# Kernel optimization log

Hardware: AMD Instinct MI355X
Metric: run time of the kernel (lower is better)

## Reference

```python
import jax, jax.numpy as jnp
import numpy as np

EMBED_DIM = 768
NUM_HEADS = 12
PROJ_DIM = EMBED_DIM // NUM_HEADS
B, S = 8, 512
PRIOR_VAR = 0.01
LOG_PRIOR_VAR = float(np.log(PRIOR_VAR))


def _kl_regularizer(w_mu, w_sigma):
    # kl_loss broadcasts [in,units] mu against [units] logvar, then mean over all
    kl_loss = (LOG_PRIOR_VAR - 1.0 - w_sigma
               + jnp.log1p(jnp.exp(w_sigma)) / PRIOR_VAR
               + jnp.square(w_mu) / PRIOR_VAR)
    return 0.5 * jnp.mean(kl_loss)


def _linear_not_first(mu_in, Sigma_in, w_mu, w_sigma):
    in_dim = jnp.float32(w_mu.shape[0])
    units = jnp.float32(w_mu.shape[1])
    x_dim = jnp.float32(mu_in.shape[-1])
    mu_out = mu_in @ w_mu
    kl = _kl_regularizer(w_mu, w_sigma)
    W_Sigma = jnp.log1p(jnp.exp(w_sigma))  # softplus, shape [units]
    # w_t_Sigma_i_w: (w_mu/sqrt(in_dim))^2 = w_mu^2/in_dim
    Sigma_1 = Sigma_in @ (jnp.square(w_mu) / in_dim)
    # x_Sigma_w_x_T: x/x_dim, then sum(x*x) * W_Sigma
    xs = mu_in / x_dim
    xx_t = jnp.sum(xs * xs, axis=-1, keepdims=True)
    Sigma_2 = xx_t * W_Sigma
    # tr_Sigma_w_Sigma_in
    Sigma_3 = jnp.sum(Sigma_in, axis=-1, keepdims=True) * W_Sigma / units
    Sigma_out = jax.nn.softplus(Sigma_1 + Sigma_2 + Sigma_3)
    return mu_out, Sigma_out, kl


def _separate_heads(x):
    # [B,S,E] -> [B,H,S,d]
    return x.reshape(B, S, NUM_HEADS, PROJ_DIM).transpose(0, 2, 1, 3)


def _attention(mu_q, sg_q, mu_k, sg_k, mu_v, sg_v):
    dk = jnp.float32(PROJ_DIM)
    mu_score = jnp.einsum('bhqd,bhkd->bhqk', mu_q, mu_k)
    a = jnp.einsum('bhqd,bhkd->bhqk', jnp.square(mu_q) / dk, sg_k)
    # NOTE: faithful to TF source: matmul(mu_key^2/dk, sigma_query, transpose_b)
    b = jnp.einsum('bhkd,bhqd->bhkq', jnp.square(mu_k) / dk, sg_q)
    c = jnp.einsum('bhqd,bhkd->bhqk', sg_q, sg_k) / dk
    sigma_score = a + b + c
    mu_scaled = mu_score / jnp.sqrt(dk)
    sigma_scaled = sigma_score / dk
    mu_w = jax.nn.softmax(mu_scaled, axis=-1)
    wd = jnp.float32(mu_w.shape[-1])
    grad = jnp.square(mu_w - jnp.square(mu_w))
    Sigma_w = grad * sigma_scaled / wd
    mu_out = jnp.einsum('bhqk,bhkd->bhqd', mu_w, mu_v)
    d = jnp.einsum('bhqk,bhkd->bhqd', jnp.square(mu_w) / wd, sg_v)
    e = jnp.einsum('bhqk,bhkd->bhqd', Sigma_w, jnp.square(mu_v) / wd)
    f = jnp.einsum('bhqk,bhkd->bhqd', Sigma_w, sg_v) / wd
    return mu_out, jax.nn.softplus(d + e + f)


def _forward(mu_inputs, sigma_inputs, wq_mu, wq_sigma, wk_mu, wk_sigma,
             wv_mu, wv_sigma, wo_mu, wo_sigma):
    # eval mode: VDP_Dropout is identity
    mu_q, sg_q, kl_q = _linear_not_first(mu_inputs, sigma_inputs, wq_mu, wq_sigma)
    mu_k, sg_k, kl_k = _linear_not_first(mu_inputs, sigma_inputs, wk_mu, wk_sigma)
    mu_v, sg_v, kl_v = _linear_not_first(mu_inputs, sigma_inputs, wv_mu, wv_sigma)
    mu_q, sg_q = _separate_heads(mu_q), _separate_heads(sg_q)
    mu_k, sg_k = _separate_heads(mu_k), _separate_heads(sg_k)
    mu_v, sg_v = _separate_heads(mu_v), _separate_heads(sg_v)
    mu_att, sg_att = _attention(mu_q, sg_q, mu_k, sg_k, mu_v, sg_v)
    mu_cat = mu_att.transpose(0, 2, 1, 3).reshape(B, S, EMBED_DIM)
    sg_cat = sg_att.transpose(0, 2, 1, 3).reshape(B, S, EMBED_DIM)
    mu_out, Sigma_out, kl_o = _linear_not_first(mu_cat, sg_cat, wo_mu, wo_sigma)
    kl = kl_q + kl_k + kl_v + kl_o
    return mu_out, Sigma_out, kl


def setup_inputs() -> dict:
    key = jax.random.key(0)
    ks = jax.random.split(key, 10)
    glorot = float(np.sqrt(2.0 / (EMBED_DIM + EMBED_DIM)))
    def w_pair(k1, k2):
        w_mu = jax.random.normal(k1, (EMBED_DIM, EMBED_DIM), jnp.float32) * glorot
        w_sigma = jax.random.uniform(k2, (EMBED_DIM,), jnp.float32,
                                     minval=-4.6, maxval=-2.25)
        return w_mu, w_sigma
    wq_mu, wq_sigma = w_pair(ks[0], ks[1])
    wk_mu, wk_sigma = w_pair(ks[2], ks[3])
    wv_mu, wv_sigma = w_pair(ks[4], ks[5])
    wo_mu, wo_sigma = w_pair(ks[6], ks[7])
    mu_inputs = jax.random.normal(ks[8], (B, S, EMBED_DIM), jnp.float32)
    sigma_inputs = jax.random.uniform(ks[9], (B, S, EMBED_DIM), jnp.float32)
    return {"mu_inputs": mu_inputs, "sigma_inputs": sigma_inputs,
            "wq_mu": wq_mu, "wq_sigma": wq_sigma,
            "wk_mu": wk_mu, "wk_sigma": wk_sigma,
            "wv_mu": wv_mu, "wv_sigma": wv_sigma,
            "wo_mu": wo_mu, "wo_sigma": wo_sigma}


def reference(mu_inputs, sigma_inputs, wq_mu, wq_sigma, wk_mu, wk_sigma,
              wv_mu, wv_sigma, wo_mu, wo_sigma):
    return _forward(mu_inputs, sigma_inputs, wq_mu, wq_sigma, wk_mu, wk_sigma,
                    wv_mu, wv_sigma, wo_mu, wo_sigma)
```

## Files before the change

### kernel.cpp

```cpp
#include <hip/hip_runtime.h>
#include <math.h>

constexpr int E = 768;
constexpr int H = 12;
constexpr int D = 64;
constexpr int Bsz = 8;
constexpr int S = 512;
constexpr int NROWS = Bsz * S;
constexpr float LOG_PV_M1 = -5.605170185988091f;
constexpr float INV_PV = 100.0f;

typedef __attribute__((ext_vector_type(8))) short short8;
typedef __attribute__((ext_vector_type(4))) float floatx4;

__device__ __forceinline__ float softplusf(float x) {
    return fmaxf(x, 0.f) + log1pf(expf(-fabsf(x)));
}
__device__ __forceinline__ unsigned short f2bf(float f) {
    unsigned int u = __float_as_uint(f);
    unsigned int r = (u + 0x7fffu + ((u >> 16) & 1u)) >> 16;
    return (unsigned short)r;
}
__device__ __forceinline__ float bf2f(unsigned short h) {
    return __uint_as_float(((unsigned int)h) << 16);
}
__device__ __forceinline__ unsigned int pack2(float a, float b) {
    return (unsigned int)f2bf(a) | ((unsigned int)f2bf(b) << 16);
}
__device__ __forceinline__ void split2(float a, float b, unsigned int& hi, unsigned int& lo) {
    unsigned short ha = f2bf(a), hb = f2bf(b);
    hi = (unsigned int)ha | ((unsigned int)hb << 16);
    lo = (unsigned int)f2bf(a - bf2f(ha)) | ((unsigned int)f2bf(b - bf2f(hb)) << 16);
}

__global__ void zero_kernel(float* p) { if (threadIdx.x == 0) p[0] = 0.f; }

__global__ __launch_bounds__(256) void kl_kernel(const float* __restrict__ wmu,
                                                 const float* __restrict__ wsig,
                                                 float* __restrict__ out) {
    int tid = blockIdx.x * 256 + threadIdx.x;
    int nthr = gridDim.x * 256;
    float partial = 0.f;
    for (int i = tid; i < E * E; i += nthr) {
        float w = wmu[i];
        partial += w * w;
    }
    partial *= INV_PV;
    if (tid < E) {
        float ws = wsig[tid];
        partial += (float)E * (LOG_PV_M1 - ws + softplusf(ws) * INV_PV);
    }
    __shared__ float red[256];
    red[threadIdx.x] = partial;
    __syncthreads();
    for (int s = 128; s > 0; s >>= 1) {
        if (threadIdx.x < s) red[threadIdx.x] += red[threadIdx.x + s];
        __syncthreads();
    }
    if (threadIdx.x == 0)
        atomicAdd(out, 0.5f * red[0] / (float)(E * E));
}

__global__ __launch_bounds__(256) void rowstats_kernel(const float* __restrict__ mu,
                                                       const float* __restrict__ sg,
                                                       float* __restrict__ xx,
                                                       float* __restrict__ ss) {
    int wave = threadIdx.x >> 6, lane = threadIdx.x & 63;
    int row = blockIdx.x * 4 + wave;
    const float* mrow = mu + (size_t)row * E;
    const float* srow = sg + (size_t)row * E;
    float s2 = 0.f, s1 = 0.f;
    for (int i = lane; i < E; i += 64) {
        float m = mrow[i];
        s2 += m * m;
        s1 += srow[i];
    }
    for (int off = 32; off > 0; off >>= 1) {
        s2 += __shfl_xor(s2, off);
        s1 += __shfl_xor(s1, off);
    }
    if (lane == 0) {
        xx[row] = s2 * (1.f / ((float)E * (float)E));
        ss[row] = s1;
    }
}

__global__ __launch_bounds__(512, 1) void linear_mfma_kernel(
    const float* __restrict__ Amu, const float* __restrict__ Asg,
    const float* __restrict__ Wmu, const float* __restrict__ wsig,
    const float* __restrict__ xx, const float* __restrict__ ss,
    float* __restrict__ Cmu, float* __restrict__ Csg) {
    constexpr int BM = 64, BN = 128, BK = 32, LDK = 40;
    __shared__ unsigned short A_mu[BM][LDK], A_sg[BM][LDK];
    __shared__ unsigned short W_mu[BN][LDK], W_sg[BN][LDK];
    const int m0 = blockIdx.x * BM;
    const int n0 = blockIdx.y * BN;
    const int t = threadIdx.x;
    const int lane = t & 63, wid = t >> 6;
    const int qsub = wid >> 1, c2 = wid & 1;
    const int lr = lane & 15, lg = lane >> 4;

    floatx4 accm[4] = {{0.f,0.f,0.f,0.f},{0.f,0.f,0.f,0.f},{0.f,0.f,0.f,0.f},{0.f,0.f,0.f,0.f}};
    floatx4 accs[4] = {{0.f,0.f,0.f,0.f},{0.f,0.f,0.f,0.f},{0.f,0.f,0.f,0.f},{0.f,0.f,0.f,0.f}};

    for (int k0 = 0; k0 < E; k0 += BK) {
        __syncthreads();
        {
            int r = t >> 3, g = (t & 7) * 4;
            float4 am = *(const float4*)&Amu[(size_t)(m0 + r) * E + k0 + g];
            float4 as = *(const float4*)&Asg[(size_t)(m0 + r) * E + k0 + g];
            *(uint2*)&A_mu[r][g] = make_uint2(pack2(am.x, am.y), pack2(am.z, am.w));
            *(uint2*)&A_sg[r][g] = make_uint2(pack2(as.x, as.y), pack2(as.z, as.w));
        }
        {
            int kp = t & 15, n4 = (t >> 4) * 4;
            const float* p0 = &Wmu[(size_t)(k0 + 2 * kp) * E + n0 + n4];
            const float* p1 = p0 + E;
            float4 w0 = *(const float4*)p0, w1 = *(const float4*)p1;
            *(unsigned int*)&W_mu[n4 + 0][2 * kp] = pack2(w0.x, w1.x);
            *(unsigned int*)&W_mu[n4 + 1][2 * kp] = pack2(w0.y, w1.y);
            *(unsigned int*)&W_mu[n4 + 2][2 * kp] = pack2(w0.z, w1.z);
            *(unsigned int*)&W_mu[n4 + 3][2 * kp] = pack2(w0.w, w1.w);
            const float is = 1.f / 768.f;
            *(unsigned int*)&W_sg[n4 + 0][2 * kp] = pack2(w0.x * w0.x * is, w1.x * w1.x * is);
            *(unsigned int*)&W_sg[n4 + 1][2 * kp] = pack2(w0.y * w0.y * is, w1.y * w1.y * is);
            *(unsigned int*)&W_sg[n4 + 2][2 * kp] = pack2(w0.z * w0.z * is, w1.z * w1.z * is);
            *(unsigned int*)&W_sg[n4 + 3][2 * kp] = pack2(w0.w * w0.w * is, w1.w * w1.w * is);
        }
        __syncthreads();
        short8 a_mu = *(const short8*)&A_mu[qsub * 16 + lr][lg * 8];
        short8 a_sg = *(const short8*)&A_sg[qsub * 16 + lr][lg * 8];
#pragma unroll
        for (int f = 0; f < 4; ++f) {
            int col = c2 * 64 + f * 16 + lr;
            short8 b_mu = *(const short8*)&W_mu[col][lg * 8];
            short8 b_sg = *(const short8*)&W_sg[col][lg * 8];
            accm[f] = __builtin_amdgcn_mfma_f32_16x16x32_bf16(a_mu, b_mu, accm[f], 0, 0, 0);
            accs[f] = __builtin_amdgcn_mfma_f32_16x16x32_bf16(a_sg, b_sg, accs[f], 0, 0, 0);
        }
    }
#pragma unroll
    for (int f = 0; f < 4; ++f) {
        int n = n0 + c2 * 64 + f * 16 + lr;
        float WS = softplusf(wsig[n]);
#pragma unroll
        for (int v = 0; v < 4; ++v) {
            int m = m0 + qsub * 16 + lg * 4 + v;
            Cmu[(size_t)m * E + n] = accm[f][v];
            float sg = accs[f][v] + xx[m] * WS + ss[m] * WS * (1.f / 768.f);
            Csg[(size_t)m * E + n] = softplusf(sg);
        }
    }
}

__global__ __launch_bounds__(512, 1) void attn_mfma_kernel(
    const float* __restrict__ mu_q, const float* __restrict__ sg_q,
    const float* __restrict__ mu_k, const float* __restrict__ sg_k,
    const float* __restrict__ mu_v, const float* __restrict__ sg_v,
    float* __restrict__ mu_o, float* __restrict__ sg_o) {
    constexpr int QB = 64, KC = 64, LDK = 72;
    __shared__ unsigned short q_hi[QB][LDK], q_lo[QB][LDK], q_cb[QB][LDK], q_k2[QB][LDK];
    __shared__ unsigned short k_hi[KC][LDK], k_lo[KC][LDK], k_sg[KC][LDK], k_qsg[KC][LDK];
    __shared__ unsigned short vT_mu[D][LDK], vT_sg[D][LDK], vT_cb[D][LDK];
    __shared__ unsigned short p_w[QB][LDK], p_w2[QB][LDK], p_sw[QB][LDK];
    __shared__ float red_m[2][QB], red_z[2][QB];

    const int bid = blockIdx.x;
    const int qt = bid & 7;
    const int hb = bid >> 3;
    const int h = hb % H;
    const int b = hb / H;
    const int q0 = qt * QB;
    const int t = threadIdx.x;
    const int lane = t & 63, wid = t >> 6;
    const int qsub = wid >> 1, c2 = wid & 1;
    const int Q0 = qsub * 16;
    const int lr = lane & 15, lg = lane >> 4;
    const size_t base = (size_t)b * S * E + (size_t)h * D;

    {
        int r = t >> 3, g = (t & 7) * 8;
        const float* pm = mu_q + base + (size_t)(q0 + r) * E + g;
        const float* ps = sg_q + base + (size_t)(q0 + r) * E + g;
        const float* pk = mu_k + base + (size_t)(q0 + r) * E + g;
        float4 m0 = *(const float4*)pm, m1 = *(const float4*)(pm + 4);
        float4 s0 = *(const float4*)ps, s1 = *(const float4*)(ps + 4);
        float4 k0 = *(const float4*)pk, k1 = *(const float4*)(pk + 4);
        unsigned int h0, l0, h1, l1, h2, l2, h3, l3;
        split2(m0.x, m0.y, h0, l0); split2(m0.z, m0.w, h1, l1);
        split2(m1.x, m1.y, h2, l2); split2(m1.z, m1.w, h3, l3);
        *(uint4*)&q_hi[r][g] = make_uint4(h0, h1, h2, h3);
        *(uint4*)&q_lo[r][g] = make_uint4(l0, l1, l2, l3);
        const float i64 = 1.f / 64.f;
        *(uint4*)&q_cb[r][g] = make_uint4(
            pack2((m0.x * m0.x + s0.x) * i64, (m0.y * m0.y + s0.y) * i64),
            pack2((m0.z * m0.z + s0.z) * i64, (m0.w * m0.w + s0.w) * i64),
            pack2((m1.x * m1.x + s1.x) * i64, (m1.y * m1.y + s1.y) * i64),
            pack2((m1.z * m1.z + s1.z) * i64, (m1.w * m1.w + s1.w) * i64));
        *(uint4*)&q_k2[r][g] = make_uint4(
            pack2(k0.x * k0.x * i64, k0.y * k0.y * i64),
            pack2(k0.z * k0.z * i64, k0.w * k0.w * i64),
            pack2(k1.x * k1.x * i64, k1.y * k1.y * i64),
            pack2(k1.z * k1.z * i64, k1.w * k1.w * i64));
    }

    float mv[4], zv[4];
#pragma unroll
    for (int v = 0; v < 4; ++v) { mv[v] = -1e30f; zv[v] = 0.f; }

    for (int c = 0; c < S / KC; ++c) {
        __syncthreads();
        {
            int r = t >> 3, g = (t & 7) * 8;
            const float* pk = mu_k + base + (size_t)(c * KC + r) * E + g;
            float4 k0 = *(const float4*)pk, k1 = *(const float4*)(pk + 4);
            unsigned int h0, l0, h1, l1, h2, l2, h3, l3;
            split2(k0.x, k0.y, h0, l0); split2(k0.z, k0.w, h1, l1);
            split2(k1.x, k1.y, h2, l2); split2(k1.z, k1.w, h3, l3);
            *(uint4*)&k_hi[r][g] = make_uint4(h0, h1, h2, h3);
            *(uint4*)&k_lo[r][g] = make_uint4(l0, l1, l2, l3);
        }
        __syncthreads();
        floatx4 cm[2] = {{0.f, 0.f, 0.f, 0.f}, {0.f, 0.f, 0.f, 0.f}};
#pragma unroll
        for (int ks = 0; ks < 2; ++ks) {
            int ao = lg * 8 + ks * 32;
            short8 ahi = *(const short8*)&q_hi[Q0 + lr][ao];
            short8 alo = *(const short8*)&q_lo[Q0 + lr][ao];
#pragma unroll
            for (int f = 0; f < 2; ++f) {
                int key = c2 * 32 + f * 16 + lr;
                short8 bhi = *(const short8*)&k_hi[key][ao];
                short8 blo = *(const short8*)&k_lo[key][ao];
                cm[f] = __builtin_amdgcn_mfma_f32_16x16x32_bf16(ahi, bhi, cm[f], 0, 0, 0);
                cm[f] = __builtin_amdgcn_mfma_f32_16x16x32_bf16(ahi, blo, cm[f], 0, 0, 0);
                cm[f] = __builtin_amdgcn_mfma_f32_16x16x32_bf16(alo, bhi, cm[f], 0, 0, 0);
            }
        }
#pragma unroll
        for (int v = 0; v < 4; ++v) {
            float s0 = cm[0][v] * 0.125f, s1 = cm[1][v] * 0.125f;
            float cmx = fmaxf(s0, s1);
            for (int off = 1; off <= 8; off <<= 1) cmx = fmaxf(cmx, __shfl_xor(cmx, off));
            float ez = __expf(s0 - cmx) + __expf(s1 - cmx);
            for (int off = 1; off <= 8; off <<= 1) ez += __shfl_xor(ez, off);
            float nm = fmaxf(mv[v], cmx);
            zv[v] = zv[v] * __expf(mv[v] - nm) + ez * __expf(cmx - nm);
            mv[v] = nm;
        }
    }
    __syncthreads();
    if ((lane & 15) == 0) {
#pragma unroll
        for (int v = 0; v < 4; ++v) {
            int qr = Q0 + lg * 4 + v;
            red_m[c2][qr] = mv[v];
            red_z[c2][qr] = zv[v];
        }
    }
    __syncthreads();
    float fm[4], fzi[4];
#pragma unroll
    for (int v = 0; v < 4; ++v) {
        int qr = Q0 + lg * 4 + v;
        float m0 = red_m[0][qr], m1 = red_m[1][qr];
        float mm = fmaxf(m0, m1);
        float zz = red_z[0][qr] * __expf(m0 - mm) + red_z[1][qr] * __expf(m1 - mm);
        fm[v] = mm;
        fzi[v] = 1.f / zz;
    }

    floatx4 accm[2] = {{0.f, 0.f, 0.f, 0.f}, {0.f, 0.f, 0.f, 0.f}};
    floatx4 accs[2] = {{0.f, 0.f, 0.f, 0.f}, {0.f, 0.f, 0.f, 0.f}};
    for (int c = 0; c < S / KC; ++c) {
        __syncthreads();
        {
            int r = t >> 3, g = (t & 7) * 8;
            const float* pk = mu_k + base + (size_t)(c * KC + r) * E + g;
            const float* pskk = sg_k + base + (size_t)(c * KC + r) * E + g;
            const float* psq = sg_q + base + (size_t)(c * KC + r) * E + g;
            float4 k0 = *(const float4*)pk, k1 = *(const float4*)(pk + 4);
            float4 s0 = *(const float4*)pskk, s1 = *(const float4*)(pskk + 4);
            float4 g0 = *(const float4*)psq, g1 = *(const float4*)(psq + 4);
            unsigned int h0, l0, h1, l1, h2, l2, h3, l3;
            split2(k0.x, k0.y, h0, l0); split2(k0.z, k0.w, h1, l1);
            split2(k1.x, k1.y, h2, l2); split2(k1.z, k1.w, h3, l3);
            *(uint4*)&k_hi[r][g] = make_uint4(h0, h1, h2, h3);
            *(uint4*)&k_lo[r][g] = make_uint4(l0, l1, l2, l3);
            *(uint4*)&k_sg[r][g] = make_uint4(pack2(s0.x, s0.y), pack2(s0.z, s0.w),
                                              pack2(s1.x, s1.y), pack2(s1.z, s1.w));
            *(uint4*)&k_qsg[r][g] = make_uint4(pack2(g0.x, g0.y), pack2(g0.z, g0.w),
                                               pack2(g1.x, g1.y), pack2(g1.z, g1.w));
        }
        {
            int kp = t & 31, dg = (t >> 5) * 4;
            const float* pv0 = mu_v + base + (size_t)(c * KC + 2 * kp) * E + dg;
            const float* pv1 = pv0 + E;
            const float* ps0 = sg_v + base + (size_t)(c * KC + 2 * kp) * E + dg;
            const float* ps1 = ps0 + E;
            float4 a0 = *(const float4*)pv0, a1 = *(const float4*)pv1;
            float4 b0 = *(const float4*)ps0, b1 = *(const float4*)ps1;
            *(unsigned int*)&vT_mu[dg + 0][2 * kp] = pack2(a0.x, a1.x);
            *(unsigned int*)&vT_mu[dg + 1][2 * kp] = pack2(a0.y, a1.y);
            *(unsigned int*)&vT_mu[dg + 2][2 * kp] = pack2(a0.z, a1.z);
            *(unsigned int*)&vT_mu[dg + 3][2 * kp] = pack2(a0.w, a1.w);
            *(unsigned int*)&vT_sg[dg + 0][2 * kp] = pack2(b0.x, b1.x);
            *(unsigned int*)&vT_sg[dg + 1][2 * kp] = pack2(b0.y, b1.y);
            *(unsigned int*)&vT_sg[dg + 2][2 * kp] = pack2(b0.z, b1.z);
            *(unsigned int*)&vT_sg[dg + 3][2 * kp] = pack2(b0.w, b1.w);
            *(unsigned int*)&vT_cb[dg + 0][2 * kp] = pack2(a0.x * a0.x + b0.x, a1.x * a1.x + b1.x);
            *(unsigned int*)&vT_cb[dg + 1][2 * kp] = pack2(a0.y * a0.y + b0.y, a1.y * a1.y + b1.y);
            *(unsigned int*)&vT_cb[dg + 2][2 * kp] = pack2(a0.z * a0.z + b0.z, a1.z * a1.z + b1.z);
            *(unsigned int*)&vT_cb[dg + 3][2 * kp] = pack2(a0.w * a0.w + b0.w, a1.w * a1.w + b1.w);
        }
        __syncthreads();
        floatx4 cm[2] = {{0.f, 0.f, 0.f, 0.f}, {0.f, 0.f, 0.f, 0.f}};
        floatx4 cs[2] = {{0.f, 0.f, 0.f, 0.f}, {0.f, 0.f, 0.f, 0.f}};
#pragma unroll
        for (int ks = 0; ks < 2; ++ks) {
            int ao = lg * 8 + ks * 32;
            short8 ahi = *(const short8*)&q_hi[Q0 + lr][ao];
            short8 alo = *(const short8*)&q_lo[Q0 + lr][ao];
            short8 acb = *(const short8*)&q_cb[Q0 + lr][ao];
            short8 ak2 = *(const short8*)&q_k2[Q0 + lr][ao];
#pragma unroll
            for (int f = 0; f < 2; ++f) {
                int key = c2 * 32 + f * 16 + lr;
                short8 bhi = *(const short8*)&k_hi[key][ao];
                short8 blo = *(const short8*)&k_lo[key][ao];
                short8 bsg = *(const short8*)&k_sg[key][ao];
                short8 bqs = *(const short8*)&k_qsg[key][ao];
                cm[f] = __builtin_amdgcn_mfma_f32_16x16x32_bf16(ahi, bhi, cm[f], 0, 0, 0);
                cm[f] = __builtin_amdgcn_mfma_f32_16x16x32_bf16(ahi, blo, cm[f], 0, 0, 0);
                cm[f] = __builtin_amdgcn_mfma_f32_16x16x32_bf16(alo, bhi, cm[f], 0, 0, 0);
                cs[f] = __builtin_amdgcn_mfma_f32_16x16x32_bf16(acb, bsg, cs[f], 0, 0, 0);
                cs[f] = __builtin_amdgcn_mfma_f32_16x16x32_bf16(ak2, bqs, cs[f], 0, 0, 0);
            }
        }
#pragma unroll
        for (int f = 0; f < 2; ++f)
#pragma unroll
            for (int v = 0; v < 4; ++v) {
                int qr = Q0 + lg * 4 + v;
                int key = c2 * 32 + f * 16 + lr;
                float w = __expf(cm[f][v] * 0.125f - fm[v]) * fzi[v];
                float sgs = cs[f][v] * (1.f / 64.f);
                float g1 = w - w * w;
                p_w[qr][key] = f2bf(w);
                p_w2[qr][key] = f2bf(w * w * (1.f / 512.f));
                p_sw[qr][key] = f2bf(g1 * g1 * sgs * (1.f / 262144.f));
            }
        __syncthreads();
#pragma unroll
        for (int ks = 0; ks < 2; ++ks) {
            int ko = lg * 8 + ks * 32;
            short8 aw = *(const short8*)&p_w[Q0 + lr][ko];
            short8 aw2 = *(const short8*)&p_w2[Q0 + lr][ko];
            short8 asw = *(const short8*)&p_sw[Q0 + lr][ko];
#pragma unroll
            for (int nf = 0; nf < 2; ++nf) {
                int dcol = (wid & 1) * 32 + nf * 16 + lr;
                short8 bvm = *(const short8*)&vT_mu[dcol][ko];
                short8 bvs = *(const short8*)&vT_sg[dcol][ko];
                short8 bvc = *(const short8*)&vT_cb[dcol][ko];
                accm[nf] = __builtin_amdgcn_mfma_f32_16x16x32_bf16(aw, bvm, accm[nf], 0, 0, 0);
                accs[nf] = __builtin_amdgcn_mfma_f32_16x16x32_bf16(aw2, bvs, accs[nf], 0, 0, 0);
                accs[nf] = __builtin_amdgcn_mfma_f32_16x16x32_bf16(asw, bvc, accs[nf], 0, 0, 0);
            }
        }
    }
#pragma unroll
    for (int nf = 0; nf < 2; ++nf)
#pragma unroll
        for (int v = 0; v < 4; ++v) {
            int qg = q0 + Q0 + lg * 4 + v;
            int dcol = (wid & 1) * 32 + nf * 16 + lr;
            size_t g = base + (size_t)qg * E + dcol;
            mu_o[g] = accm[nf][v];
            sg_o[g] = softplusf(accs[nf][v]);
        }
}

extern "C" void kernel_launch(void* const* d_in, const int* in_sizes, int n_in,
                              void* d_out, int out_size, void* d_ws, size_t ws_size,
                              hipStream_t stream) {
    const float* mu_in = (const float*)d_in[0];
    const float* sg_in = (const float*)d_in[1];
    const float* wq_mu = (const float*)d_in[2];
    const float* wq_sg = (const float*)d_in[3];
    const float* wk_mu = (const float*)d_in[4];
    const float* wk_sg = (const float*)d_in[5];
    const float* wv_mu = (const float*)d_in[6];
    const float* wv_sg = (const float*)d_in[7];
    const float* wo_mu = (const float*)d_in[8];
    const float* wo_sg = (const float*)d_in[9];

    float* out_mu = (float*)d_out;
    float* out_sg = out_mu + (size_t)NROWS * E;
    float* out_kl = out_sg + (size_t)NROWS * E;

    const size_t NE = (size_t)NROWS * E;
    float* ws = (float*)d_ws;
    float* mu_q = ws;
    float* sg_q = ws + NE;
    float* mu_k = ws + 2 * NE;
    float* sg_k = ws + 3 * NE;
    float* mu_v = ws + 4 * NE;
    float* sg_v = ws + 5 * NE;
    float* mu_a = ws + 6 * NE;
    float* sg_a = ws + 7 * NE;
    float* xx = ws + 8 * NE;
    float* ss = xx + NROWS;
    float* xx2 = ss + NROWS;
    float* ss2 = xx2 + NROWS;

    zero_kernel<<<1, 64, 0, stream>>>(out_kl);
    kl_kernel<<<64, 256, 0, stream>>>(wq_mu, wq_sg, out_kl);
    kl_kernel<<<64, 256, 0, stream>>>(wk_mu, wk_sg, out_kl);
    kl_kernel<<<64, 256, 0, stream>>>(wv_mu, wv_sg, out_kl);
    kl_kernel<<<64, 256, 0, stream>>>(wo_mu, wo_sg, out_kl);

    rowstats_kernel<<<NROWS / 4, 256, 0, stream>>>(mu_in, sg_in, xx, ss);

    dim3 ggrid(NROWS / 64, E / 128);
    linear_mfma_kernel<<<ggrid, 512, 0, stream>>>(mu_in, sg_in, wq_mu, wq_sg, xx, ss, mu_q, sg_q);
    linear_mfma_kernel<<<ggrid, 512, 0, stream>>>(mu_in, sg_in, wk_mu, wk_sg, xx, ss, mu_k, sg_k);
    linear_mfma_kernel<<<ggrid, 512, 0, stream>>>(mu_in, sg_in, wv_mu, wv_sg, xx, ss, mu_v, sg_v);

    attn_mfma_kernel<<<Bsz * H * (S / 64), 512, 0, stream>>>(mu_q, sg_q, mu_k, sg_k,
                                                             mu_v, sg_v, mu_a, sg_a);

    rowstats_kernel<<<NROWS / 4, 256, 0, stream>>>(mu_a, sg_a, xx2, ss2);
    linear_mfma_kernel<<<ggrid, 512, 0, stream>>>(mu_a, sg_a, wo_mu, wo_sg, xx2, ss2, out_mu, out_sg);
}
```

Baseline: 540.4 us.

## Pre-pack inputs, weights and intermediates to bf16 in producer epilogues

Inputs and transposed weights (plus squared/scaled weight variants) are converted to bf16 once in dedicated pack kernels. The Q/K/V linear epilogues now write attention-ready bf16 planes (hi/lo splits, sigma, mu^2+sigma), and attention writes bf16 outputs consumed by a bf16 rowstats and the output projection. This is meant to halve intermediate memory traffic and remove repeated conversion and transposition work inside the GEMM and attention inner loops. In exchange it adds extra launches and storage of more planes, and the output projection now reads bf16-rounded attention outputs, which may reduce accuracy slightly.

```diff
diff --git a/kernel.cpp b/kernel.cpp
--- a/kernel.cpp
+++ b/kernel.cpp
@@ -7,6 +7,8 @@
 constexpr int Bsz = 8;
 constexpr int S = 512;
 constexpr int NROWS = Bsz * S;
+constexpr int NE_ = NROWS * E;
+constexpr int WE = E * E;
 constexpr float LOG_PV_M1 = -5.605170185988091f;
 constexpr float INV_PV = 100.0f;
 
@@ -26,11 +28,6 @@
 }
 __device__ __forceinline__ unsigned int pack2(float a, float b) {
     return (unsigned int)f2bf(a) | ((unsigned int)f2bf(b) << 16);
-}
-__device__ __forceinline__ void split2(float a, float b, unsigned int& hi, unsigned int& lo) {
-    unsigned short ha = f2bf(a), hb = f2bf(b);
-    hi = (unsigned int)ha | ((unsigned int)hb << 16);
-    lo = (unsigned int)f2bf(a - bf2f(ha)) | ((unsigned int)f2bf(b - bf2f(hb)) << 16);
 }
 
 __global__ void zero_kernel(float* p) { if (threadIdx.x == 0) p[0] = 0.f; }
@@ -59,6 +56,49 @@
     }
     if (threadIdx.x == 0)
         atomicAdd(out, 0.5f * red[0] / (float)(E * E));
+}
+
+__global__ __launch_bounds__(256) void pack_in_kernel(const float* __restrict__ mu,
+                                                      const float* __restrict__ sg,
+                                                      unsigned short* __restrict__ m16,
+                                                      unsigned short* __restrict__ s16) {
+    size_t i = ((size_t)blockIdx.x * 256 + threadIdx.x) * 8;
+    float4 a0 = *(const float4*)(mu + i);
+    float4 a1 = *(const float4*)(mu + i + 4);
+    *(uint4*)(m16 + i) = make_uint4(pack2(a0.x, a0.y), pack2(a0.z, a0.w),
+                                    pack2(a1.x, a1.y), pack2(a1.z, a1.w));
+    float4 b0 = *(const float4*)(sg + i);
+    float4 b1 = *(const float4*)(sg + i + 4);
+    *(uint4*)(s16 + i) = make_uint4(pack2(b0.x, b0.y), pack2(b0.z, b0.w),
+                                    pack2(b1.x, b1.y), pack2(b1.z, b1.w));
+}
+
+__global__ __launch_bounds__(256) void packT_kernel(
+    const float* __restrict__ w0, const float* __restrict__ w1,
+    const float* __restrict__ w2, const float* __restrict__ w3,
+    unsigned short* __restrict__ wtm, unsigned short* __restrict__ wts) {
+    const float* W = (blockIdx.z == 0) ? w0 : (blockIdx.z == 1) ? w1
+                   : (blockIdx.z == 2) ? w2 : w3;
+    unsigned short* om = wtm + (size_t)blockIdx.z * WE;
+    unsigned short* os = wts + (size_t)blockIdx.z * WE;
+    __shared__ float tile[32][33];
+    int k0 = blockIdx.x * 32, n0 = blockIdx.y * 32;
+    int t = threadIdx.x;
+    {
+        int r = t >> 3, c = (t & 7) * 4;
+        float4 v = *(const float4*)&W[(size_t)(k0 + r) * E + n0 + c];
+        tile[r][c] = v.x; tile[r][c + 1] = v.y; tile[r][c + 2] = v.z; tile[r][c + 3] = v.w;
+    }
+    __syncthreads();
+    {
+        int n = t >> 3, r = (t & 7) * 4;
+        float v0 = tile[r][n], v1 = tile[r + 1][n], v2 = tile[r + 2][n], v3 = tile[r + 3][n];
+        size_t o = (size_t)(n0 + n) * E + k0 + r;
+        *(uint2*)&om[o] = make_uint2(pack2(v0, v1), pack2(v2, v3));
+        const float is = 1.f / 768.f;
+        *(uint2*)&os[o] = make_uint2(pack2(v0 * v0 * is, v1 * v1 * is),
+                                     pack2(v2 * v2 * is, v3 * v3 * is));
+    }
 }
 
 __global__ __launch_bounds__(256) void rowstats_kernel(const float* __restrict__ mu,
@@ -85,47 +125,66 @@
     }
 }
 
-__global__ __launch_bounds__(512, 1) void linear_mfma_kernel(
-    const float* __restrict__ Amu, const float* __restrict__ Asg,
-    const float* __restrict__ Wmu, const float* __restrict__ wsig,
-    const float* __restrict__ xx, const float* __restrict__ ss,
-    float* __restrict__ Cmu, float* __restrict__ Csg) {
-    constexpr int BM = 64, BN = 128, BK = 32, LDK = 40;
-    __shared__ unsigned short A_mu[BM][LDK], A_sg[BM][LDK];
-    __shared__ unsigned short W_mu[BN][LDK], W_sg[BN][LDK];
-    const int m0 = blockIdx.x * BM;
-    const int n0 = blockIdx.y * BN;
-    const int t = threadIdx.x;
-    const int lane = t & 63, wid = t >> 6;
+__global__ __launch_bounds__(256) void rowstats16_kernel(const unsigned short* __restrict__ m16,
+                                                         const unsigned short* __restrict__ s16,
+                                                         float* __restrict__ xx,
+                                                         float* __restrict__ ss) {
+    int wave = threadIdx.x >> 6, lane = threadIdx.x & 63;
+    int row = blockIdx.x * 4 + wave;
+    const unsigned short* mrow = m16 + (size_t)row * E;
+    const unsigned short* srow = s16 + (size_t)row * E;
+    float s2 = 0.f, s1 = 0.f;
+    for (int c = lane; c < 96; c += 64) {
+        uint4 um = *(const uint4*)(mrow + c * 8);
+        uint4 us = *(const uint4*)(srow + c * 8);
+        unsigned int mw[4] = {um.x, um.y, um.z, um.w};
+        unsigned int sw[4] = {us.x, us.y, us.z, us.w};
+#pragma unroll
+        for (int j = 0; j < 4; ++j) {
+            float a = bf2f((unsigned short)(mw[j] & 0xffff));
+            float b = bf2f((unsigned short)(mw[j] >> 16));
+            s2 += a * a + b * b;
+            s1 += bf2f((unsigned short)(sw[j] & 0xffff)) + bf2f((unsigned short)(sw[j] >> 16));
+        }
+    }
+    for (int off = 32; off > 0; off >>= 1) {
+        s2 += __shfl_xor(s2, off);
+        s1 += __shfl_xor(s1, off);
+    }
+    if (lane == 0) {
+        xx[row] = s2 * (1.f / ((float)E * (float)E));
+        ss[row] = s1;
+    }
+}
+
+template <int ROLE>
+__global__ __launch_bounds__(512, 1) void linear2_kernel(
+    const unsigned short* __restrict__ A16m, const unsigned short* __restrict__ A16s,
+    const unsigned short* __restrict__ WTm, const unsigned short* __restrict__ WTs,
+    const float* __restrict__ wsig, const float* __restrict__ xx, const float* __restrict__ ss,
+    void* __restrict__ o0v, void* __restrict__ o1v, void* __restrict__ o2v) {
+    constexpr int LDK = 40;
+    __shared__ unsigned short A_mu[64][LDK], A_sg[64][LDK];
+    __shared__ unsigned short W_mu[128][LDK], W_sg[128][LDK];
+    const int m0 = blockIdx.x * 64, n0 = blockIdx.y * 128;
+    const int t = threadIdx.x, lane = t & 63, wid = t >> 6;
     const int qsub = wid >> 1, c2 = wid & 1;
     const int lr = lane & 15, lg = lane >> 4;
 
     floatx4 accm[4] = {{0.f,0.f,0.f,0.f},{0.f,0.f,0.f,0.f},{0.f,0.f,0.f,0.f},{0.f,0.f,0.f,0.f}};
     floatx4 accs[4] = {{0.f,0.f,0.f,0.f},{0.f,0.f,0.f,0.f},{0.f,0.f,0.f,0.f},{0.f,0.f,0.f,0.f}};
 
-    for (int k0 = 0; k0 < E; k0 += BK) {
+    for (int k0 = 0; k0 < E; k0 += 32) {
         __syncthreads();
         {
-            int r = t >> 3, g = (t & 7) * 4;
-            float4 am = *(const float4*)&Amu[(size_t)(m0 + r) * E + k0 + g];
-            float4 as = *(const float4*)&Asg[(size_t)(m0 + r) * E + k0 + g];
-            *(uint2*)&A_mu[r][g] = make_uint2(pack2(am.x, am.y), pack2(am.z, am.w));
-            *(uint2*)&A_sg[r][g] = make_uint2(pack2(as.x, as.y), pack2(as.z, as.w));
+            int r = t >> 3, c = (t & 7) * 4;
+            *(uint2*)&A_mu[r][c] = *(const uint2*)(A16m + (size_t)(m0 + r) * E + k0 + c);
+            *(uint2*)&A_sg[r][c] = *(const uint2*)(A16s + (size_t)(m0 + r) * E + k0 + c);
         }
         {
-            int kp = t & 15, n4 = (t >> 4) * 4;
-            const float* p0 = &Wmu[(size_t)(k0 + 2 * kp) * E + n0 + n4];
-            const float* p1 = p0 + E;
-            float4 w0 = *(const float4*)p0, w1 = *(const float4*)p1;
-            *(unsigned int*)&W_mu[n4 + 0][2 * kp] = pack2(w0.x, w1.x);
-            *(unsigned int*)&W_mu[n4 + 1][2 * kp] = pack2(w0.y, w1.y);
-            *(unsigned int*)&W_mu[n4 + 2][2 * kp] = pack2(w0.z, w1.z);
-            *(unsigned int*)&W_mu[n4 + 3][2 * kp] = pack2(w0.w, w1.w);
-            const float is = 1.f / 768.f;
-            *(unsigned int*)&W_sg[n4 + 0][2 * kp] = pack2(w0.x * w0.x * is, w1.x * w1.x * is);
-            *(unsigned int*)&W_sg[n4 + 1][2 * kp] = pack2(w0.y * w0.y * is, w1.y * w1.y * is);
-            *(unsigned int*)&W_sg[n4 + 2][2 * kp] = pack2(w0.z * w0.z * is, w1.z * w1.z * is);
-            *(unsigned int*)&W_sg[n4 + 3][2 * kp] = pack2(w0.w * w0.w * is, w1.w * w1.w * is);
+            int n = t >> 2, c = (t & 3) * 8;
+            *(uint4*)&W_mu[n][c] = *(const uint4*)(WTm + (size_t)(n0 + n) * E + k0 + c);
+            *(uint4*)&W_sg[n][c] = *(const uint4*)(WTs + (size_t)(n0 + n) * E + k0 + c);
         }
         __syncthreads();
         short8 a_mu = *(const short8*)&A_mu[qsub * 16 + lr][lg * 8];
@@ -146,18 +205,34 @@
 #pragma unroll
         for (int v = 0; v < 4; ++v) {
             int m = m0 + qsub * 16 + lg * 4 + v;
-            Cmu[(size_t)m * E + n] = accm[f][v];
-            float sg = accs[f][v] + xx[m] * WS + ss[m] * WS * (1.f / 768.f);
-            Csg[(size_t)m * E + n] = softplusf(sg);
-        }
-    }
-}
-
-__global__ __launch_bounds__(512, 1) void attn_mfma_kernel(
-    const float* __restrict__ mu_q, const float* __restrict__ sg_q,
-    const float* __restrict__ mu_k, const float* __restrict__ sg_k,
-    const float* __restrict__ mu_v, const float* __restrict__ sg_v,
-    float* __restrict__ mu_o, float* __restrict__ sg_o) {
+            size_t off = (size_t)m * E + n;
+            float mu = accm[f][v];
+            float sgo = softplusf(accs[f][v] + xx[m] * WS + ss[m] * WS * (1.f / 768.f));
+            if (ROLE == 0) {
+                unsigned short hi = f2bf(mu);
+                ((unsigned short*)o0v)[off] = hi;
+                ((unsigned short*)o1v)[off] = f2bf(mu - bf2f(hi));
+                ((unsigned short*)o2v)[off] = f2bf(sgo);
+            } else if (ROLE == 1) {
+                ((unsigned short*)o0v)[off] = f2bf(mu);
+                ((unsigned short*)o1v)[off] = f2bf(sgo);
+                ((unsigned short*)o2v)[off] = f2bf(mu * mu + sgo);
+            } else {
+                ((float*)o0v)[off] = mu;
+                ((float*)o1v)[off] = sgo;
+            }
+        }
+    }
+}
+
+__global__ __launch_bounds__(512, 1) void attn2_kernel(
+    const unsigned short* __restrict__ q_hi_g, const unsigned short* __restrict__ q_lo_g,
+    const unsigned short* __restrict__ q_sg_g,
+    const unsigned short* __restrict__ k_hi_g, const unsigned short* __restrict__ k_lo_g,
+    const unsigned short* __restrict__ k_sg_g,
+    const unsigned short* __restrict__ v_mu_g, const unsigned short* __restrict__ v_sg_g,
+    const unsigned short* __restrict__ v_cb_g,
+    unsigned short* __restrict__ a_m16, unsigned short* __restrict__ a_s16) {
     constexpr int QB = 64, KC = 64, LDK = 72;
     __shared__ unsigned short q_hi[QB][LDK], q_lo[QB][LDK], q_cb[QB][LDK], q_k2[QB][LDK];
     __shared__ unsigned short k_hi[KC][LDK], k_lo[KC][LDK], k_sg[KC][LDK], k_qsg[KC][LDK];
@@ -180,28 +255,34 @@
 
     {
         int r = t >> 3, g = (t & 7) * 8;
-        const float* pm = mu_q + base + (size_t)(q0 + r) * E + g;
-        const float* ps = sg_q + base + (size_t)(q0 + r) * E + g;
-        const float* pk = mu_k + base + (size_t)(q0 + r) * E + g;
-        float4 m0 = *(const float4*)pm, m1 = *(const float4*)(pm + 4);
-        float4 s0 = *(const float4*)ps, s1 = *(const float4*)(ps + 4);
-        float4 k0 = *(const float4*)pk, k1 = *(const float4*)(pk + 4);
-        unsigned int h0, l0, h1, l1, h2, l2, h3, l3;
-        split2(m0.x, m0.y, h0, l0); split2(m0.z, m0.w, h1, l1);
-        split2(m1.x, m1.y, h2, l2); split2(m1.z, m1.w, h3, l3);
-        *(uint4*)&q_hi[r][g] = make_uint4(h0, h1, h2, h3);
-        *(uint4*)&q_lo[r][g] = make_uint4(l0, l1, l2, l3);
+        size_t off = base + (size_t)(q0 + r) * E + g;
+        uint4 hi4 = *(const uint4*)(q_hi_g + off);
+        uint4 lo4 = *(const uint4*)(q_lo_g + off);
+        uint4 sg4 = *(const uint4*)(q_sg_g + off);
+        uint4 kh4 = *(const uint4*)(k_hi_g + off);
+        uint4 kl4 = *(const uint4*)(k_lo_g + off);
+        *(uint4*)&q_hi[r][g] = hi4;
+        *(uint4*)&q_lo[r][g] = lo4;
+        unsigned int hw[4] = {hi4.x, hi4.y, hi4.z, hi4.w};
+        unsigned int lw[4] = {lo4.x, lo4.y, lo4.z, lo4.w};
+        unsigned int sw[4] = {sg4.x, sg4.y, sg4.z, sg4.w};
+        unsigned int khw[4] = {kh4.x, kh4.y, kh4.z, kh4.w};
+        unsigned int klw[4] = {kl4.x, kl4.y, kl4.z, kl4.w};
+        unsigned int cbw[4], k2w[4];
         const float i64 = 1.f / 64.f;
-        *(uint4*)&q_cb[r][g] = make_uint4(
-            pack2((m0.x * m0.x + s0.x) * i64, (m0.y * m0.y + s0.y) * i64),
-            pack2((m0.z * m0.z + s0.z) * i64, (m0.w * m0.w + s0.w) * i64),
-            pack2((m1.x * m1.x + s1.x) * i64, (m1.y * m1.y + s1.y) * i64),
-            pack2((m1.z * m1.z + s1.z) * i64, (m1.w * m1.w + s1.w) * i64));
-        *(uint4*)&q_k2[r][g] = make_uint4(
-            pack2(k0.x * k0.x * i64, k0.y * k0.y * i64),
-            pack2(k0.z * k0.z * i64, k0.w * k0.w * i64),
-            pack2(k1.x * k1.x * i64, k1.y * k1.y * i64),
-            pack2(k1.z * k1.z * i64, k1.w * k1.w * i64));
+#pragma unroll
+        for (int j = 0; j < 4; ++j) {
+            float m0f = bf2f((unsigned short)(hw[j] & 0xffff)) + bf2f((unsigned short)(lw[j] & 0xffff));
+            float m1f = bf2f((unsigned short)(hw[j] >> 16)) + bf2f((unsigned short)(lw[j] >> 16));
+            float s0f = bf2f((unsigned short)(sw[j] & 0xffff));
+            float s1f = bf2f((unsigned short)(sw[j] >> 16));
+            cbw[j] = pack2((m0f * m0f + s0f) * i64, (m1f * m1f + s1f) * i64);
+            float km0 = bf2f((unsigned short)(khw[j] & 0xffff)) + bf2f((unsigned short)(klw[j] & 0xffff));
+            float km1 = bf2f((unsigned short)(khw[j] >> 16)) + bf2f((unsigned short)(klw[j] >> 16));
+            k2w[j] = pack2(km0 * km0 * i64, km1 * km1 * i64);
+        }
+        *(uint4*)&q_cb[r][g] = make_uint4(cbw[0], cbw[1], cbw[2], cbw[3]);
+        *(uint4*)&q_k2[r][g] = make_uint4(k2w[0], k2w[1], k2w[2], k2w[3]);
     }
 
     float mv[4], zv[4];
@@ -212,13 +293,9 @@
         __syncthreads();
         {
             int r = t >> 3, g = (t & 7) * 8;
-            const float* pk = mu_k + base + (size_t)(c * KC + r) * E + g;
-            float4 k0 = *(const float4*)pk, k1 = *(const float4*)(pk + 4);
-            unsigned int h0, l0, h1, l1, h2, l2, h3, l3;
-            split2(k0.x, k0.y, h0, l0); split2(k0.z, k0.w, h1, l1);
-            split2(k1.x, k1.y, h2, l2); split2(k1.z, k1.w, h3, l3);
-            *(uint4*)&k_hi[r][g] = make_uint4(h0, h1, h2, h3);
-            *(uint4*)&k_lo[r][g] = make_uint4(l0, l1, l2, l3);
+            size_t off = base + (size_t)(c * KC + r) * E + g;
+            *(uint4*)&k_hi[r][g] = *(const uint4*)(k_hi_g + off);
+            *(uint4*)&k_lo[r][g] = *(const uint4*)(k_lo_g + off);
         }
         __syncthreads();
         floatx4 cm[2] = {{0.f, 0.f, 0.f, 0.f}, {0.f, 0.f, 0.f, 0.f}};
@@ -276,42 +353,31 @@
         __syncthreads();
         {
             int r = t >> 3, g = (t & 7) * 8;
-            const float* pk = mu_k + base + (size_t)(c * KC + r) * E + g;
-            const float* pskk = sg_k + base + (size_t)(c * KC + r) * E + g;
-            const float* psq = sg_q + base + (size_t)(c * KC + r) * E + g;
-            float4 k0 = *(const float4*)pk, k1 = *(const float4*)(pk + 4);
-            float4 s0 = *(const float4*)pskk, s1 = *(const float4*)(pskk + 4);
-            float4 g0 = *(const float4*)psq, g1 = *(const float4*)(psq + 4);
-            unsigned int h0, l0, h1, l1, h2, l2, h3, l3;
-            split2(k0.x, k0.y, h0, l0); split2(k0.z, k0.w, h1, l1);
-            split2(k1.x, k1.y, h2, l2); split2(k1.z, k1.w, h3, l3);
-            *(uint4*)&k_hi[r][g] = make_uint4(h0, h1, h2, h3);
-            *(uint4*)&k_lo[r][g] = make_uint4(l0, l1, l2, l3);
-            *(uint4*)&k_sg[r][g] = make_uint4(pack2(s0.x, s0.y), pack2(s0.z, s0.w),
-                                              pack2(s1.x, s1.y), pack2(s1.z, s1.w));
-            *(uint4*)&k_qsg[r][g] = make_uint4(pack2(g0.x, g0.y), pack2(g0.z, g0.w),
-                                               pack2(g1.x, g1.y), pack2(g1.z, g1.w));
+            size_t off = base + (size_t)(c * KC + r) * E + g;
+            *(uint4*)&k_hi[r][g] = *(const uint4*)(k_hi_g + off);
+            *(uint4*)&k_lo[r][g] = *(const uint4*)(k_lo_g + off);
+            *(uint4*)&k_sg[r][g] = *(const uint4*)(k_sg_g + off);
+            *(uint4*)&k_qsg[r][g] = *(const uint4*)(q_sg_g + off);
         }
         {
             int kp = t & 31, dg = (t >> 5) * 4;
-            const float* pv0 = mu_v + base + (size_t)(c * KC + 2 * kp) * E + dg;
-            const float* pv1 = pv0 + E;
-            const float* ps0 = sg_v + base + (size_t)(c * KC + 2 * kp) * E + dg;
-            const float* ps1 = ps0 + E;
-            float4 a0 = *(const float4*)pv0, a1 = *(const float4*)pv1;
-            float4 b0 = *(const float4*)ps0, b1 = *(const float4*)ps1;
-            *(unsigned int*)&vT_mu[dg + 0][2 * kp] = pack2(a0.x, a1.x);
-            *(unsigned int*)&vT_mu[dg + 1][2 * kp] = pack2(a0.y, a1.y);
-            *(unsigned int*)&vT_mu[dg + 2][2 * kp] = pack2(a0.z, a1.z);
-            *(unsigned int*)&vT_mu[dg + 3][2 * kp] = pack2(a0.w, a1.w);
-            *(unsigned int*)&vT_sg[dg + 0][2 * kp] = pack2(b0.x, b1.x);
-            *(unsigned int*)&vT_sg[dg + 1][2 * kp] = pack2(b0.y, b1.y);
-            *(unsigned int*)&vT_sg[dg + 2][2 * kp] = pack2(b0.z, b1.z);
-            *(unsigned int*)&vT_sg[dg + 3][2 * kp] = pack2(b0.w, b1.w);
-            *(unsigned int*)&vT_cb[dg + 0][2 * kp] = pack2(a0.x * a0.x + b0.x, a1.x * a1.x + b1.x);
-            *(unsigned int*)&vT_cb[dg + 1][2 * kp] = pack2(a0.y * a0.y + b0.y, a1.y * a1.y + b1.y);
-            *(unsigned int*)&vT_cb[dg + 2][2 * kp] = pack2(a0.z * a0.z + b0.z, a1.z * a1.z + b1.z);
-            *(unsigned int*)&vT_cb[dg + 3][2 * kp] = pack2(a0.w * a0.w + b0.w, a1.w * a1.w + b1.w);
+            size_t o0 = base + (size_t)(c * KC + 2 * kp) * E + dg;
+            size_t o1 = o0 + E;
+            uint2 am = *(const uint2*)(v_mu_g + o0), bm = *(const uint2*)(v_mu_g + o1);
+            uint2 as_ = *(const uint2*)(v_sg_g + o0), bs_ = *(const uint2*)(v_sg_g + o1);
+            uint2 ac = *(const uint2*)(v_cb_g + o0), bc = *(const uint2*)(v_cb_g + o1);
+            *(unsigned int*)&vT_mu[dg + 0][2 * kp] = (am.x & 0xffffu) | (bm.x << 16);
+            *(unsigned int*)&vT_mu[dg + 1][2 * kp] = (am.x >> 16) | (bm.x & 0xffff0000u);
+            *(unsigned int*)&vT_mu[dg + 2][2 * kp] = (am.y & 0xffffu) | (bm.y << 16);
+            *(unsigned int*)&vT_mu[dg + 3][2 * kp] = (am.y >> 16) | (bm.y & 0xffff0000u);
+            *(unsigned int*)&vT_sg[dg + 0][2 * kp] = (as_.x & 0xffffu) | (bs_.x << 16);
+            *(unsigned int*)&vT_sg[dg + 1][2 * kp] = (as_.x >> 16) | (bs_.x & 0xffff0000u);
+            *(unsigned int*)&vT_sg[dg + 2][2 * kp] = (as_.y & 0xffffu) | (bs_.y << 16);
+            *(unsigned int*)&vT_sg[dg + 3][2 * kp] = (as_.y >> 16) | (bs_.y & 0xffff0000u);
+            *(unsigned int*)&vT_cb[dg + 0][2 * kp] = (ac.x & 0xffffu) | (bc.x << 16);
+            *(unsigned int*)&vT_cb[dg + 1][2 * kp] = (ac.x >> 16) | (bc.x & 0xffff0000u);
+            *(unsigned int*)&vT_cb[dg + 2][2 * kp] = (ac.y & 0xffffu) | (bc.y << 16);
+            *(unsigned int*)&vT_cb[dg + 3][2 * kp] = (ac.y >> 16) | (bc.y & 0xffff0000u);
         }
         __syncthreads();
         floatx4 cm[2] = {{0.f, 0.f, 0.f, 0.f}, {0.f, 0.f, 0.f, 0.f}};
@@ -376,8 +442,8 @@
             int qg = q0 + Q0 + lg * 4 + v;
             int dcol = (wid & 1) * 32 + nf * 16 + lr;
             size_t g = base + (size_t)qg * E + dcol;
-            mu_o[g] = accm[nf][v];
-            sg_o[g] = softplusf(accs[nf][v]);
+            a_m16[g] = f2bf(accm[nf][v]);
+            a_s16[g] = f2bf(softplusf(accs[nf][v]));
         }
 }
 
@@ -396,23 +462,30 @@
     const float* wo_sg = (const float*)d_in[9];
 
     float* out_mu = (float*)d_out;
-    float* out_sg = out_mu + (size_t)NROWS * E;
-    float* out_kl = out_sg + (size_t)NROWS * E;
-
-    const size_t NE = (size_t)NROWS * E;
-    float* ws = (float*)d_ws;
-    float* mu_q = ws;
-    float* sg_q = ws + NE;
-    float* mu_k = ws + 2 * NE;
-    float* sg_k = ws + 3 * NE;
-    float* mu_v = ws + 4 * NE;
-    float* sg_v = ws + 5 * NE;
-    float* mu_a = ws + 6 * NE;
-    float* sg_a = ws + 7 * NE;
-    float* xx = ws + 8 * NE;
-    float* ss = xx + NROWS;
-    float* xx2 = ss + NROWS;
-    float* ss2 = xx2 + NROWS;
+    float* out_sg = out_mu + (size_t)NE_;
+    float* out_kl = out_sg + (size_t)NE_;
+
+    unsigned short* sp = (unsigned short*)d_ws;
+    unsigned short* in_m16 = sp;
+    unsigned short* in_s16 = sp + (size_t)NE_;
+    unsigned short* q_hi = sp + 2 * (size_t)NE_;
+    unsigned short* q_lo = sp + 3 * (size_t)NE_;
+    unsigned short* q_sg = sp + 4 * (size_t)NE_;
+    unsigned short* k_hi = sp + 5 * (size_t)NE_;
+    unsigned short* k_lo = sp + 6 * (size_t)NE_;
+    unsigned short* k_sg = sp + 7 * (size_t)NE_;
+    unsigned short* v_mu = sp + 8 * (size_t)NE_;
+    unsigned short* v_sg = sp + 9 * (size_t)NE_;
+    unsigned short* v_cb = sp + 10 * (size_t)NE_;
+    unsigned short* a_m16 = sp + 11 * (size_t)NE_;
+    unsigned short* a_s16 = sp + 12 * (size_t)NE_;
+    unsigned short* wt_mu = sp + 13 * (size_t)NE_;
+    unsigned short* wt_sg = wt_mu + 4 * (size_t)WE;
+    float* fstats = (float*)(wt_sg + 4 * (size_t)WE);
+    float* xx = fstats;
+    float* ss = fstats + NROWS;
+    float* xx2 = fstats + 2 * NROWS;
+    float* ss2 = fstats + 3 * NROWS;
 
     zero_kernel<<<1, 64, 0, stream>>>(out_kl);
     kl_kernel<<<64, 256, 0, stream>>>(wq_mu, wq_sg, out_kl);
@@ -420,16 +493,22 @@
     kl_kernel<<<64, 256, 0, stream>>>(wv_mu, wv_sg, out_kl);
     kl_kernel<<<64, 256, 0, stream>>>(wo_mu, wo_sg, out_kl);
 
+    pack_in_kernel<<<NE_ / 2048, 256, 0, stream>>>(mu_in, sg_in, in_m16, in_s16);
+    packT_kernel<<<dim3(24, 24, 4), 256, 0, stream>>>(wq_mu, wk_mu, wv_mu, wo_mu, wt_mu, wt_sg);
     rowstats_kernel<<<NROWS / 4, 256, 0, stream>>>(mu_in, sg_in, xx, ss);
 
     dim3 ggrid(NROWS / 64, E / 128);
-    linear_mfma_kernel<<<ggrid, 512, 0, stream>>>(mu_in, sg_in, wq_mu, wq_sg, xx, ss, mu_q, sg_q);
-    linear_mfma_kernel<<<ggrid, 512, 0, stream>>>(mu_in, sg_in, wk_mu, wk_sg, xx, ss, mu_k, sg_k);
-    linear_mfma_kernel<<<ggrid, 512, 0, stream>>>(mu_in, sg_in, wv_mu, wv_sg, xx, ss, mu_v, sg_v);
-
-    attn_mfma_kernel<<<Bsz * H * (S / 64), 512, 0, stream>>>(mu_q, sg_q, mu_k, sg_k,
-                                                             mu_v, sg_v, mu_a, sg_a);
-
-    rowstats_kernel<<<NROWS / 4, 256, 0, stream>>>(mu_a, sg_a, xx2, ss2);
-    linear_mfma_kernel<<<ggrid, 512, 0, stream>>>(mu_a, sg_a, wo_mu, wo_sg, xx2, ss2, out_mu, out_sg);
-}
+    linear2_kernel<0><<<ggrid, 512, 0, stream>>>(in_m16, in_s16, wt_mu, wt_sg,
+                                                 wq_sg, xx, ss, q_hi, q_lo, q_sg);
+    linear2_kernel<0><<<ggrid, 512, 0, stream>>>(in_m16, in_s16, wt_mu + (size_t)WE, wt_sg + (size_t)WE,
+                                                 wk_sg, xx, ss, k_hi, k_lo, k_sg);
+    linear2_kernel<1><<<ggrid, 512, 0, stream>>>(in_m16, in_s16, wt_mu + 2 * (size_t)WE, wt_sg + 2 * (size_t)WE,
+                                                 wv_sg, xx, ss, v_mu, v_sg, v_cb);
+
+    attn2_kernel<<<Bsz * H * (S / 64), 512, 0, stream>>>(q_hi, q_lo, q_sg, k_hi, k_lo, k_sg,
+                                                         v_mu, v_sg, v_cb, a_m16, a_s16);
+
+    rowstats16_kernel<<<NROWS / 4, 256, 0, stream>>>(a_m16, a_s16, xx2, ss2);
+    linear2_kernel<2><<<ggrid, 512, 0, stream>>>(a_m16, a_s16, wt_mu + 3 * (size_t)WE, wt_sg + 3 * (size_t)WE,
+                                                 wo_sg, xx2, ss2, out_mu, out_sg, nullptr);
+}
```

Result: faster. 514.0 us (-4.9%).
